# Kernel optimization log

Measured on AMD Instinct MI355X. Metric: run time of the kernel, lower is better.

The kernel has to match this reference:

```python
import jax, jax.numpy as jnp
import numpy as np

NUM_HEADS = 16


def setup_inputs() -> dict:
    key = jax.random.key(0)
    k1, k2, k3 = jax.random.split(key, 3)
    S, B, E = 2048, 4, 1024
    std = float(np.sqrt(2.0 / (E + E)))
    query = jax.random.normal(k1, (S, B, E), dtype=jnp.float32)
    in_proj_weight = jax.random.normal(k2, (3 * E, E), dtype=jnp.float32) * std
    in_proj_bias = jnp.zeros((3 * E,), dtype=jnp.float32)
    out_proj_weight = jax.random.normal(k3, (E, E), dtype=jnp.float32) * std
    out_proj_bias = jnp.zeros((E,), dtype=jnp.float32)
    return {
        "query": query,
        "in_proj_weight": in_proj_weight,
        "in_proj_bias": in_proj_bias,
        "out_proj_weight": out_proj_weight,
        "out_proj_bias": out_proj_bias,
    }


def reference(query, in_proj_weight, in_proj_bias, out_proj_weight, out_proj_bias):
    S, B, E = query.shape
    H = NUM_HEADS
    hd = E // H
    scale = hd ** -0.5
    # fused QKV projection: [S, B, 3E]
    lin = jnp.einsum("sbe,fe->sbf", query, in_proj_weight) + in_proj_bias
    # torch layout: view(S, B*H, 3, hd) -> interleaved [h, {q,k,v}, hd]
    lin = lin.reshape(S, B * H, 3, hd)
    q = lin[:, :, 0, :]  # [S, B*H, hd]
    k = lin[:, :, 1, :]
    v = lin[:, :, 2, :]
    # scores: [B*H, S_q, S_k]
    scores = jnp.einsum("sbd,tbd->bst", q, k) * scale
    attn = jax.nn.softmax(scores.astype(jnp.float32), axis=-1).astype(scores.dtype)
    # context: [S, B*H, hd] -> [S, B, E]
    ctx = jnp.einsum("bst,tbd->sbd", attn, v).reshape(S, B, E)
    out = jnp.einsum("sbe,fe->sbf", ctx, out_proj_weight) + out_proj_bias
    return out
```

## Files before the change

kernel.cpp:

```cpp
#include <hip/hip_runtime.h>
#include <hip/hip_bf16.h>

typedef __hip_bfloat16 bf16;
typedef __attribute__((ext_vector_type(8))) short short8;
typedef __attribute__((ext_vector_type(4))) float floatx4;

#define GLD_LDS(g, l) __builtin_amdgcn_global_load_lds( \
    (const __attribute__((address_space(1))) void*)(g), \
    (__attribute__((address_space(3))) void*)(l), 16, 0, 0)

#define CS 0.18033688f

__device__ __forceinline__ float fast_exp2(float x)
{
    const float fl = floorf(x);
    const float t  = x - fl;
    float p = 1.0f + t * (0.69583f + t * (0.22606f + t * 0.078024f));
    union { float f; int i; } u;
    u.f = p;
    u.i += ((int)fl) << 23;
    return u.f;
}

__global__ __launch_bounds__(256)
void cvt3_kernel(const float* __restrict__ q,  bf16* __restrict__ qo,
                 const float* __restrict__ w1, bf16* __restrict__ w1o,
                 const float* __restrict__ w2, bf16* __restrict__ w2o)
{
    const int i = blockIdx.x * 256 + threadIdx.x;
    const float* src; bf16* dst; long off;
    if (i < 1048576)       { src = q;  dst = qo;  off = (long)i * 8; }
    else if (i < 1441792)  { src = w1; dst = w1o; off = (long)(i - 1048576) * 8; }
    else                   { src = w2; dst = w2o; off = (long)(i - 1441792) * 8; }
    floatx4 a = *(const floatx4*)(src + off);
    floatx4 b = *(const floatx4*)(src + off + 4);
    short8 h;
    #pragma unroll
    for (int e = 0; e < 4; ++e) {
        union { bf16 v; short s; } u0, u1;
        u0.v = __float2bfloat16(a[e]); h[e]     = u0.s;
        u1.v = __float2bfloat16(b[e]); h[e + 4] = u1.s;
    }
    *(short8*)(dst + off) = h;
}

__device__ __forceinline__ void stage_f32(const float* __restrict__ src, int ld,
                                          bf16* lds, int t)
{
    const int sr = t >> 1;
    const int sc = (t & 1) * 16;
    const float* g = src + (long)sr * ld + sc;
    floatx4 f[4];
    #pragma unroll
    for (int i = 0; i < 4; ++i) f[i] = *(const floatx4*)(g + i * 4);
    short8 h[2];
    #pragma unroll
    for (int v = 0; v < 2; ++v)
        #pragma unroll
        for (int e = 0; e < 8; ++e) {
            union { bf16 b; short s; } u;
            u.b = __float2bfloat16(f[v * 2 + (e >> 2)][e & 3]);
            h[v][e] = u.s;
        }
    *(short8*)(lds + sr * 32 + sc)     = h[0];
    *(short8*)(lds + sr * 32 + sc + 8) = h[1];
}

template<int EPI, int AF32, int BF32>
__global__ __launch_bounds__(256, 2)
void gemm_bt(const void* __restrict__ Ap, const void* __restrict__ Bp,
             const float* __restrict__ bias,
             void* __restrict__ o0, bf16* __restrict__ o1, bf16* __restrict__ o2,
             int K, int N)
{
    __shared__ __align__(16) bf16 lA[128 * 32];
    __shared__ __align__(16) bf16 lB[128 * 32];

    const int t    = threadIdx.x;
    const int lane = t & 63;
    const int w    = t >> 6;

    const int nb   = N >> 7;
    const int lin  = blockIdx.y * nb + blockIdx.x;
    const int cpx  = (nb << 6) >> 3;
    const int swz  = (lin & 7) * cpx + (lin >> 3);
    const int mBase = (swz / nb) * 128;
    const int nBase = (swz % nb) * 128;

    const int wr = (w >> 1) * 64;
    const int wc = (w & 1) * 64;

    const int rowL = t >> 2;
    const int colL = (t & 3) * 8;
    const bf16* gA0 = (const bf16*)Ap + (long)(mBase + rowL) * K + colL;
    const bf16* gA1 = (const bf16*)Ap + (long)(mBase + rowL + 64) * K + colL;
    const bf16* gB0 = (const bf16*)Bp + (long)(nBase + rowL) * K + colL;
    const bf16* gB1 = (const bf16*)Bp + (long)(nBase + rowL + 64) * K + colL;
    char* lAb = (char*)lA + w * 1024;
    char* lBb = (char*)lB + w * 1024;

    floatx4 acc[4][4] = {};

    for (int k0 = 0; k0 < K; k0 += 32) {
        if constexpr (AF32) {
            stage_f32((const float*)Ap + (long)mBase * K + k0, K, lA, t);
        } else {
            GLD_LDS(gA0 + k0, lAb);
            GLD_LDS(gA1 + k0, lAb + 4096);
        }
        if constexpr (BF32) {
            stage_f32((const float*)Bp + (long)nBase * K + k0, K, lB, t);
        } else {
            GLD_LDS(gB0 + k0, lBb);
            GLD_LDS(gB1 + k0, lBb + 4096);
        }
        asm volatile("s_waitcnt vmcnt(0)" ::: "memory");
        __syncthreads();

        short8 af[4], bfr[4];
        #pragma unroll
        for (int m = 0; m < 4; ++m)
            af[m] = *(const short8*)(lA + (wr + m * 16 + (lane & 15)) * 32 + (lane >> 4) * 8);
        #pragma unroll
        for (int n = 0; n < 4; ++n)
            bfr[n] = *(const short8*)(lB + (wc + n * 16 + (lane & 15)) * 32 + (lane >> 4) * 8);
        #pragma unroll
        for (int m = 0; m < 4; ++m)
            #pragma unroll
            for (int n = 0; n < 4; ++n)
                acc[m][n] = __builtin_amdgcn_mfma_f32_16x16x32_bf16(af[m], bfr[n], acc[m][n], 0, 0, 0);
        __syncthreads();
    }

    #pragma unroll
    for (int m = 0; m < 4; ++m) {
        #pragma unroll
        for (int n = 0; n < 4; ++n) {
            const int col = nBase + wc + n * 16 + (lane & 15);
            const int r0  = mBase + wr + m * 16 + ((lane >> 4) << 2);
            const float bv = bias[col];
            if constexpr (EPI == 0) {
                const int h   = col / 192;
                const int rem = col % 192;
                const int qkv = rem >> 6;
                const int d   = rem & 63;
                #pragma unroll
                for (int j = 0; j < 4; ++j) {
                    const int r = r0 + j;
                    const int s = r >> 2;
                    const int b = r & 3;
                    const float v = acc[m][n][j] + bv;
                    if (qkv == 0)
                        ((bf16*)o0)[(((((b << 4) + h) << 11) + s) << 6) + d] =
                            __float2bfloat16(v * CS);
                    else if (qkv == 1)
                        o1[(((((b << 4) + h) << 11) + s) << 6) + d] = __float2bfloat16(v);
                    else
                        o2[((((b << 4) + h) << 17)) + (d << 11) + s] = __float2bfloat16(v);
                }
            } else {
                #pragma unroll
                for (int j = 0; j < 4; ++j)
                    ((float*)o0)[(long)(r0 + j) * N + col] = acc[m][n][j] + bv;
            }
        }
    }
}

__global__ __launch_bounds__(256, 2)
void attn_kernel(const bf16* __restrict__ Q, const bf16* __restrict__ Kg,
                 const bf16* __restrict__ Vt, bf16* __restrict__ Ctx)
{
    __shared__ __align__(16) bf16 lK[2][64 * 64];
    __shared__ __align__(16) bf16 lV[2][64 * 64];

    const int t    = threadIdx.x;
    const int lane = t & 63;
    const int w    = t >> 6;
    const int f    = lane & 15;
    const int g    = lane >> 4;
    const int lin  = blockIdx.x;
    const int bh   = (lin & 7) | (((lin >> 8) & 7) << 3);
    const int q0   = ((lin >> 3) & 31) * 64 + w * 16;
    const long hb  = (long)bh * 2048 * 64;
    const bf16* Qh = Q  + hb;
    const bf16* Kh = Kg + hb;
    const bf16* Vh = Vt + hb;

    const bf16* kSrc[2]; const bf16* vSrc[2];
    #pragma unroll
    for (int i = 0; i < 2; ++i) {
        const int X = t * 16 + i * 4096;
        const int r = X >> 7;
        const int c = (X & 127) ^ ((r & 7) << 4);
        const int sr = (r & 3) | ((r & 16) >> 2) | ((r & 12) << 1) | (r & 32);
        kSrc[i] = Kh + sr * 64 + (c >> 1);
        vSrc[i] = Vh + r * 2048 + (c >> 1);
    }
    const int ldst = w * 1024;

    const int rb0 = (f * 128 + g * 16)      ^ ((f & 7) << 4);
    const int rb1 = (f * 128 + g * 16 + 64) ^ ((f & 7) << 4);

    short8 qf[2];
    #pragma unroll
    for (int kk = 0; kk < 2; ++kk)
        qf[kk] = *(const short8*)(Qh + (q0 + f) * 64 + kk * 32 + g * 8);

    short8 ones;
    #pragma unroll
    for (int e = 0; e < 8; ++e) ones[e] = (short)0x3F80;

    floatx4 o[4] = {};
    floatx4 dn = {};

    #pragma unroll
    for (int i = 0; i < 2; ++i) {
        GLD_LDS(kSrc[i], (char*)lK[0] + ldst + i * 4096);
        GLD_LDS(vSrc[i], (char*)lV[0] + ldst + i * 4096);
    }
    asm volatile("s_waitcnt vmcnt(0)" ::: "memory");
    __syncthreads();

    auto tile = [&](const bf16* curK, const bf16* curV,
                    bf16* nxtK, bf16* nxtV, int t0) __attribute__((always_inline)) {
        if (t0 + 64 < 2048) {
            const int ko = (t0 + 64) * 64;
            const int vo = t0 + 64;
            #pragma unroll
            for (int i = 0; i < 2; ++i) {
                GLD_LDS(kSrc[i] + ko, (char*)nxtK + ldst + i * 4096);
                GLD_LDS(vSrc[i] + vo, (char*)nxtV + ldst + i * 4096);
            }
        }

        short8 kf[4][2];
        #pragma unroll
        for (int n = 0; n < 4; ++n) {
            kf[n][0] = *(const short8*)((const char*)curK + rb0 + n * 2048);
            kf[n][1] = *(const short8*)((const char*)curK + rb1 + n * 2048);
        }

        floatx4 sa2[4] = {};
        __builtin_amdgcn_s_setprio(1);
        #pragma unroll
        for (int n = 0; n < 4; ++n)
            #pragma unroll
            for (int kk = 0; kk < 2; ++kk)
                sa2[n] = __builtin_amdgcn_mfma_f32_16x16x32_bf16(kf[n][kk], qf[kk], sa2[n], 0, 0, 0);
        __builtin_amdgcn_s_setprio(0);

        short8 vf[4][2];
        #pragma unroll
        for (int n2 = 0; n2 < 4; ++n2) {
            vf[n2][0] = *(const short8*)((const char*)curV + rb0 + n2 * 2048);
            vf[n2][1] = *(const short8*)((const char*)curV + rb1 + n2 * 2048);
        }

        short8 pf[2];
        #pragma unroll
        for (int kk = 0; kk < 2; ++kk) {
            union { int i4[4]; short8 s8; } u;
            #pragma unroll
            for (int v = 0; v < 4; ++v) {
                const int n = 2 * kk + (v >> 1);
                const int e = 2 * (v & 1);
                float2 pr;
                pr.x = fast_exp2(sa2[n][e]);
                pr.y = fast_exp2(sa2[n][e + 1]);
                __hip_bfloat162 pb = __float22bfloat162_rn(pr);
                u.i4[v] = *reinterpret_cast<int*>(&pb);
            }
            pf[kk] = u.s8;
        }

        __builtin_amdgcn_s_setprio(1);
        #pragma unroll
        for (int n2 = 0; n2 < 4; ++n2)
            #pragma unroll
            for (int kk = 0; kk < 2; ++kk)
                o[n2] = __builtin_amdgcn_mfma_f32_16x16x32_bf16(pf[kk], vf[n2][kk], o[n2], 0, 0, 0);
        #pragma unroll
        for (int kk = 0; kk < 2; ++kk)
            dn = __builtin_amdgcn_mfma_f32_16x16x32_bf16(pf[kk], ones, dn, 0, 0, 0);
        __builtin_amdgcn_s_setprio(0);

        __syncthreads();
    };

    for (int t0 = 0; t0 < 2048; t0 += 128) {
        tile(lK[0], lV[0], lK[1], lV[1], t0);
        tile(lK[1], lV[1], lK[0], lV[0], t0 + 64);
    }

    const int b = bh >> 4;
    const int h = bh & 15;
    float inv[4];
    #pragma unroll
    for (int j = 0; j < 4; ++j)
        inv[j] = 1.f / dn[j];
    #pragma unroll
    for (int n2 = 0; n2 < 4; ++n2) {
        const int dim = (h << 6) + n2 * 16 + f;
        #pragma unroll
        for (int j = 0; j < 4; ++j) {
            const int srw = q0 + (g << 2) + j;
            Ctx[(((srw << 2) + b) << 10) + dim] = __float2bfloat16(o[n2][j] * inv[j]);
        }
    }
}

extern "C" void kernel_launch(void* const* d_in, const int* in_sizes, int n_in,
                              void* d_out, int out_size, void* d_ws, size_t ws_size,
                              hipStream_t stream)
{
    const float* query = (const float*)d_in[0];
    const float* wIn   = (const float*)d_in[1];
    const float* bIn   = (const float*)d_in[2];
    const float* wOut  = (const float*)d_in[3];
    const float* bOut  = (const float*)d_in[4];

    const size_t HEADSZ = (size_t)64 * 2048 * 64;
    bf16* Qws = (bf16*)d_ws;
    bf16* Kws = Qws + HEADSZ;
    bf16* Vtw = Kws + HEADSZ;
    bf16* Ctx = Vtw + HEADSZ;
    bf16* qbf = Ctx;
    if (ws_size < 4 * HEADSZ * sizeof(bf16)) return;

    const size_t NEED_BIG = (4 * HEADSZ + 3145728 + 1048576) * sizeof(bf16);
    if (ws_size >= NEED_BIG) {
        bf16* wInBf  = Ctx + HEADSZ;
        bf16* wOutBf = wInBf + 3145728;
        cvt3_kernel<<<dim3(6144), 256, 0, stream>>>(query, qbf, wIn, wInBf, wOut, wOutBf);
        gemm_bt<0, 0, 0><<<dim3(24, 64), 256, 0, stream>>>(qbf, wInBf, bIn,
                                                           Qws, Kws, Vtw, 1024, 3072);
        attn_kernel<<<dim3(2048), 256, 0, stream>>>(Qws, Kws, Vtw, Ctx);
        gemm_bt<1, 0, 0><<<dim3(8, 64), 256, 0, stream>>>(Ctx, wOutBf, bOut,
                                                          d_out, nullptr, nullptr, 1024, 1024);
    } else {
        cvt3_kernel<<<dim3(4096), 256, 0, stream>>>(query, qbf, nullptr, nullptr, nullptr, nullptr);
        gemm_bt<0, 0, 1><<<dim3(24, 64), 256, 0, stream>>>(qbf, wIn, bIn,
                                                           Qws, Kws, Vtw, 1024, 3072);
        attn_kernel<<<dim3(2048), 256, 0, stream>>>(Qws, Kws, Vtw, Ctx);
        gemm_bt<1, 0, 1><<<dim3(8, 64), 256, 0, stream>>>(Ctx, wOut, bOut,
                                                          d_out, nullptr, nullptr, 1024, 1024);
    }
}
```

Before: 229.8 us.

## Double-buffer LDS tiles in GEMM to overlap global loads with MFMA

The GEMM main loop now uses two LDS buffers per operand, so the next K-slice is fetched while MFMAs run on the current one. This hides global-load latency and removes one barrier per iteration. In exchange, LDS use doubles to 32KB per block, which may limit occupancy alongside the two-blocks launch bound. For f32 inputs the stage_f32 path converts through registers synchronously, so less of its cost overlaps.

```diff
diff --git a/kernel.cpp b/kernel.cpp
--- a/kernel.cpp
+++ b/kernel.cpp
@@ -73,8 +73,8 @@
              void* __restrict__ o0, bf16* __restrict__ o1, bf16* __restrict__ o2,
              int K, int N)
 {
-    __shared__ __align__(16) bf16 lA[128 * 32];
-    __shared__ __align__(16) bf16 lB[128 * 32];
+    __shared__ __align__(16) bf16 lA[2][128 * 32];
+    __shared__ __align__(16) bf16 lB[2][128 * 32];
 
     const int t    = threadIdx.x;
     const int lane = t & 63;
@@ -96,40 +96,55 @@
     const bf16* gA1 = (const bf16*)Ap + (long)(mBase + rowL + 64) * K + colL;
     const bf16* gB0 = (const bf16*)Bp + (long)(nBase + rowL) * K + colL;
     const bf16* gB1 = (const bf16*)Bp + (long)(nBase + rowL + 64) * K + colL;
-    char* lAb = (char*)lA + w * 1024;
-    char* lBb = (char*)lB + w * 1024;
+    const int ldst = w * 1024;
 
     floatx4 acc[4][4] = {};
 
-    for (int k0 = 0; k0 < K; k0 += 32) {
+    auto stage = [&](int buf, int k0) __attribute__((always_inline)) {
         if constexpr (AF32) {
-            stage_f32((const float*)Ap + (long)mBase * K + k0, K, lA, t);
+            stage_f32((const float*)Ap + (long)mBase * K + k0, K, lA[buf], t);
         } else {
-            GLD_LDS(gA0 + k0, lAb);
-            GLD_LDS(gA1 + k0, lAb + 4096);
+            GLD_LDS(gA0 + k0, (char*)lA[buf] + ldst);
+            GLD_LDS(gA1 + k0, (char*)lA[buf] + ldst + 4096);
         }
         if constexpr (BF32) {
-            stage_f32((const float*)Bp + (long)nBase * K + k0, K, lB, t);
+            stage_f32((const float*)Bp + (long)nBase * K + k0, K, lB[buf], t);
         } else {
-            GLD_LDS(gB0 + k0, lBb);
-            GLD_LDS(gB1 + k0, lBb + 4096);
-        }
+            GLD_LDS(gB0 + k0, (char*)lB[buf] + ldst);
+            GLD_LDS(gB1 + k0, (char*)lB[buf] + ldst + 4096);
+        }
+    };
+
+    auto compute = [&](int buf) __attribute__((always_inline)) {
+        short8 af[4], bfr[4];
+        #pragma unroll
+        for (int m = 0; m < 4; ++m)
+            af[m] = *(const short8*)(lA[buf] + (wr + m * 16 + (lane & 15)) * 32 + (lane >> 4) * 8);
+        #pragma unroll
+        for (int n = 0; n < 4; ++n)
+            bfr[n] = *(const short8*)(lB[buf] + (wc + n * 16 + (lane & 15)) * 32 + (lane >> 4) * 8);
+        #pragma unroll
+        for (int m = 0; m < 4; ++m)
+            #pragma unroll
+            for (int n = 0; n < 4; ++n)
+                acc[m][n] = __builtin_amdgcn_mfma_f32_16x16x32_bf16(af[m], bfr[n], acc[m][n], 0, 0, 0);
+    };
+
+    stage(0, 0);
+    asm volatile("s_waitcnt vmcnt(0)" ::: "memory");
+    __syncthreads();
+
+    for (int k0 = 0; k0 < K; k0 += 64) {
+        if (k0 + 32 < K) stage(1, k0 + 32);
+        compute(0);
         asm volatile("s_waitcnt vmcnt(0)" ::: "memory");
         __syncthreads();
-
-        short8 af[4], bfr[4];
-        #pragma unroll
-        for (int m = 0; m < 4; ++m)
-            af[m] = *(const short8*)(lA + (wr + m * 16 + (lane & 15)) * 32 + (lane >> 4) * 8);
-        #pragma unroll
-        for (int n = 0; n < 4; ++n)
-            bfr[n] = *(const short8*)(lB + (wc + n * 16 + (lane & 15)) * 32 + (lane >> 4) * 8);
-        #pragma unroll
-        for (int m = 0; m < 4; ++m)
-            #pragma unroll
-            for (int n = 0; n < 4; ++n)
-                acc[m][n] = __builtin_amdgcn_mfma_f32_16x16x32_bf16(af[m], bfr[n], acc[m][n], 0, 0, 0);
-        __syncthreads();
+        if (k0 + 32 < K) {
+            if (k0 + 64 < K) stage(0, k0 + 64);
+            compute(1);
+            asm volatile("s_waitcnt vmcnt(0)" ::: "memory");
+            __syncthreads();
+        }
     }
 
     #pragma unroll
```

New measurement: 230.3 us. About the same (+0.2%).
